# Kernel optimization log

Hardware: AMD Instinct MI355X
Metric: run time of the kernel (lower is better)

The kernel has to match this reference:

```python
import jax, jax.numpy as jnp
import numpy as np

NUM_HEADS = 8
LN_EPS = 1e-5

def setup_inputs() -> dict:
    key = jax.random.key(0)
    ks = jax.random.split(key, 8)
    B, C, H, W = 2, 512, 64, 64
    dim = C
    s = 1.0 / np.sqrt(dim)
    return {
        "pet_feat": jax.random.normal(ks[0], (B, C, H, W), jnp.float32),
        "ct_feat": jax.random.normal(ks[1], (B, C, H, W), jnp.float32),
        "Wq": jax.random.normal(ks[2], (dim, dim), jnp.float32) * s,
        "Wk": jax.random.normal(ks[3], (dim, dim), jnp.float32) * s,
        "Wv": jax.random.normal(ks[4], (dim, dim), jnp.float32) * s,
        "Wp": jax.random.normal(ks[5], (dim, dim), jnp.float32) * s,
        "bp": jnp.zeros((dim,), jnp.float32),
        "gamma": jnp.ones((dim,), jnp.float32),
        "beta": jnp.zeros((dim,), jnp.float32),
    }

def reference(pet_feat, ct_feat, Wq, Wk, Wv, Wp, bp, gamma, beta):
    B, C, H, W = pet_feat.shape
    L = H * W
    nh = NUM_HEADS
    hd = C // nh
    scale = hd ** (-0.5)
    # b c h w -> b (h w) c
    pet_seq = pet_feat.reshape(B, C, L).transpose(0, 2, 1)
    ct_seq = ct_feat.reshape(B, C, L).transpose(0, 2, 1)
    # linear projections (torch Linear: x @ W.T), split heads: b l (h d) -> b h l d
    q = (pet_seq @ Wq.T).reshape(B, L, nh, hd).transpose(0, 2, 1, 3)
    k = (ct_seq @ Wk.T).reshape(B, L, nh, hd).transpose(0, 2, 1, 3)
    v = (ct_seq @ Wv.T).reshape(B, L, nh, hd).transpose(0, 2, 1, 3)
    attn = jnp.einsum('bhld,bhmd->bhlm', q, k) * scale
    attn = jax.nn.softmax(attn, axis=-1)
    x = jnp.einsum('bhlm,bhmd->bhld', attn, v)
    # b h l d -> b l (h d)
    x = x.transpose(0, 2, 1, 3).reshape(B, L, C)
    x = x @ Wp.T + bp
    x = pet_seq + x
    # LayerNorm over channel dim
    mu = jnp.mean(x, axis=-1, keepdims=True)
    var = jnp.mean(jnp.square(x - mu), axis=-1, keepdims=True)
    x = (x - mu) * jax.lax.rsqrt(var + LN_EPS) * gamma + beta
    # b (h w) c -> b c h w
    return x.transpose(0, 2, 1).reshape(B, C, H, W)
```

## Files before the change

### kernel.cpp

```cpp
#include <hip/hip_runtime.h>

#define B_ 2
#define C_ 512
#define L_ 4096
#define NH 8
#define HD 64

typedef short bf16x8 __attribute__((ext_vector_type(8)));
typedef float f32x4 __attribute__((ext_vector_type(4)));
typedef unsigned short u16;
typedef unsigned short u16x8 __attribute__((ext_vector_type(8)));

static __device__ __forceinline__ u16 f2bf(float f) {
    union { float f; unsigned u; } v; v.f = f;
    unsigned u = v.u;
    u += 0x7fff + ((u >> 16) & 1);
    return (u16)(u >> 16);
}

static __device__ __forceinline__ unsigned cvtpk(float lo, float hi) {
    unsigned r;
    asm("v_cvt_pk_bf16_f32 %0, %1, %2" : "=v"(r) : "v"(lo), "v"(hi));
    return r;
}

__global__ __launch_bounds__(256) void transpose_conv_kernel(
        const float* __restrict__ pet, const float* __restrict__ ct,
        u16* __restrict__ petT, u16* __restrict__ ctT) {
    __shared__ float tile[64][65];
    int z  = blockIdx.z;
    int b  = z >> 1;
    const float* src = (z & 1) ? ct : pet;
    u16* dst         = (z & 1) ? ctT : petT;
    int c0 = blockIdx.y * 64;
    int l0 = blockIdx.x * 64;
    int t  = threadIdx.x;
    int i  = t >> 2;
    int jc = (t & 3) * 16;
    const float* sp = src + ((size_t)(b * C_ + c0 + i)) * L_ + l0 + jc;
#pragma unroll
    for (int p = 0; p < 4; ++p) {
        float4 v = *(const float4*)(sp + p * 4);
        tile[i][jc + p * 4 + 0] = v.x;
        tile[i][jc + p * 4 + 1] = v.y;
        tile[i][jc + p * 4 + 2] = v.z;
        tile[i][jc + p * 4 + 3] = v.w;
    }
    __syncthreads();
    int cc = (t & 3) * 16;
    u16* dp = dst + ((size_t)(b * L_ + l0 + i)) * C_ + c0 + cc;
    u16x8 o0, o1;
#pragma unroll
    for (int q = 0; q < 8; ++q) o0[q] = f2bf(tile[cc + q][i]);
#pragma unroll
    for (int q = 0; q < 8; ++q) o1[q] = f2bf(tile[cc + 8 + q][i]);
    *(u16x8*)(dp)     = o0;
    *(u16x8*)(dp + 8) = o1;
}

__global__ __launch_bounds__(256) void f2bf4_kernel(
        const float* __restrict__ s0, const float* __restrict__ s1,
        const float* __restrict__ s2, const float* __restrict__ s3,
        u16* __restrict__ d0, u16* __restrict__ d1,
        u16* __restrict__ d2, u16* __restrict__ d3) {
    const int n = 512 * 512;
    int idx = blockIdx.x * blockDim.x + threadIdx.x;
    int stride = gridDim.x * blockDim.x;
    for (int i = idx; i < n; i += stride) {
        d0[i] = f2bf(s0[i]);
        d1[i] = f2bf(s1[i]);
        d2[i] = f2bf(s2[i]);
        d3[i] = f2bf(s3[i]);
    }
}

__global__ __launch_bounds__(256) void gemm_nt_kernel(
        const u16* __restrict__ A, const u16* __restrict__ Bt,
        u16* __restrict__ Cm, int M, int N, int K,
        size_t aZ, size_t btZ, size_t cZ) {
    __shared__ u16 Al[64][72];
    __shared__ u16 Bl[64][72];
    A  += (size_t)blockIdx.z * aZ;
    Bt += (size_t)blockIdx.z * btZ;
    Cm += (size_t)blockIdx.z * cZ;
    int m0 = blockIdx.x * 64;
    int n0 = blockIdx.y * 64;
    int t = threadIdx.x;
    int w = t >> 6, lane = t & 63, ll = lane & 15, lh = lane >> 4;
    int moff = (w & 1) * 32, noff = (w >> 1) * 32;
    f32x4 acc[2][2] = {};
    int srow  = t >> 2;
    int skoff = (t & 3) * 16;
    const u16* Ap = A  + (size_t)(m0 + srow) * K + skoff;
    const u16* Bp = Bt + (size_t)(n0 + srow) * K + skoff;
    for (int kb = 0; kb < K; kb += 64) {
        u16x8 a0 = *(const u16x8*)(Ap + kb);
        u16x8 a1 = *(const u16x8*)(Ap + kb + 8);
        u16x8 b0 = *(const u16x8*)(Bp + kb);
        u16x8 b1 = *(const u16x8*)(Bp + kb + 8);
        *(u16x8*)&Al[srow][skoff]     = a0;
        *(u16x8*)&Al[srow][skoff + 8] = a1;
        *(u16x8*)&Bl[srow][skoff]     = b0;
        *(u16x8*)&Bl[srow][skoff + 8] = b1;
        __syncthreads();
#pragma unroll
        for (int kc = 0; kc < 2; ++kc) {
            bf16x8 af[2], bfr[2];
#pragma unroll
            for (int mf = 0; mf < 2; ++mf)
                af[mf] = *(const bf16x8*)&Al[moff + mf * 16 + ll][kc * 32 + lh * 8];
#pragma unroll
            for (int nf = 0; nf < 2; ++nf)
                bfr[nf] = *(const bf16x8*)&Bl[noff + nf * 16 + ll][kc * 32 + lh * 8];
#pragma unroll
            for (int mf = 0; mf < 2; ++mf)
#pragma unroll
                for (int nf = 0; nf < 2; ++nf)
                    acc[mf][nf] = __builtin_amdgcn_mfma_f32_16x16x32_bf16(
                        af[mf], bfr[nf], acc[mf][nf], 0, 0, 0);
        }
        __syncthreads();
    }
#pragma unroll
    for (int mf = 0; mf < 2; ++mf)
#pragma unroll
        for (int nf = 0; nf < 2; ++nf)
#pragma unroll
            for (int r = 0; r < 4; ++r) {
                int row = m0 + moff + mf * 16 + lh * 4 + r;
                int col = n0 + noff + nf * 16 + ll;
                Cm[(size_t)row * N + col] = f2bf(acc[mf][nf][r]);
            }
}

__global__ __launch_bounds__(256) void attn_kernel(
        const u16* __restrict__ q, const u16* __restrict__ k,
        const u16* __restrict__ vt, u16* __restrict__ X) {
    __shared__ u16 Kl[2][64][76];
    __shared__ u16 Vl[2][64][76];
    int l0 = blockIdx.x * 128;
    int h  = blockIdx.y;
    int b  = blockIdx.z;
    int t = threadIdx.x;
    int w = t >> 6, lane = t & 63, ll = lane & 15, lh = lane >> 4;
    const float C1 = 0.125f * 1.44269504088896340736f;
    const float M0 = 16.0f;

    bf16x8 qf[2][2];
#pragma unroll
    for (int u = 0; u < 2; ++u) {
        const u16* qp = q + ((size_t)(b * L_ + l0 + w * 32 + u * 16 + ll)) * C_
                          + h * HD + lh * 8;
        qf[u][0] = *(const bf16x8*)qp;
        qf[u][1] = *(const bf16x8*)(qp + 32);
    }
    int krow[4];
#pragma unroll
    for (int nf = 0; nf < 4; ++nf)
        krow[nf] = 32 * (nf & 1) + 4 * (nf >> 1) + 8 * (ll >> 2) + (ll & 3);

    int srow = t >> 2;
    int soff = (t & 3) * 16;
    const u16* kp = k  + ((size_t)(b * L_ + srow)) * C_ + h * HD + soff;
    const u16* vp = vt + ((size_t)(b * C_ + h * HD + srow)) * L_ + soff;

    u16x8 ka0 = *(const u16x8*)(kp);
    u16x8 ka1 = *(const u16x8*)(kp + 8);
    u16x8 va0 = *(const u16x8*)(vp);
    u16x8 va1 = *(const u16x8*)(vp + 8);
    *(u16x8*)&Kl[0][srow][soff]     = ka0;
    *(u16x8*)&Kl[0][srow][soff + 8] = ka1;
    *(u16x8*)&Vl[0][srow][soff]     = va0;
    *(u16x8*)&Vl[0][srow][soff + 8] = va1;
    kp += (size_t)64 * C_;
    vp += 64;

    f32x4 o[4][2] = {};
    float l_run[2] = {0.f, 0.f};

    int cur = 0;
    const int NT = L_ / 64;
    for (int tile = 0; tile < NT; ++tile) {
        __syncthreads();
        const bool pre = (tile < NT - 1);
        if (pre) {
            ka0 = *(const u16x8*)(kp);
            ka1 = *(const u16x8*)(kp + 8);
            va0 = *(const u16x8*)(vp);
            va1 = *(const u16x8*)(vp + 8);
            kp += (size_t)64 * C_;
            vp += 64;
        }
        bf16x8 kf[4][2], vf[4][2];
#pragma unroll
        for (int nf = 0; nf < 4; ++nf) {
            kf[nf][0] = *(const bf16x8*)&Kl[cur][krow[nf]][lh * 8];
            kf[nf][1] = *(const bf16x8*)&Kl[cur][krow[nf]][32 + lh * 8];
        }
#pragma unroll
        for (int df = 0; df < 4; ++df) {
            vf[df][0] = *(const bf16x8*)&Vl[cur][df * 16 + ll][lh * 8];
            vf[df][1] = *(const bf16x8*)&Vl[cur][df * 16 + ll][32 + lh * 8];
        }

        f32x4 s[2][4] = {};
#pragma unroll
        for (int kc = 0; kc < 2; ++kc)
#pragma unroll
            for (int nf = 0; nf < 4; ++nf)
#pragma unroll
                for (int u = 0; u < 2; ++u)
                    s[u][nf] = __builtin_amdgcn_mfma_f32_16x16x32_bf16(
                        kf[nf][kc], qf[u][kc], s[u][nf], 0, 0, 0);

        union { unsigned uu[4]; bf16x8 v; } pb[2][2];
#pragma unroll
        for (int u = 0; u < 2; ++u) {
            float ts = 0.f;
#pragma unroll
            for (int nf = 0; nf < 4; ++nf)
#pragma unroll
                for (int r = 0; r < 4; ++r) {
                    float pv = __builtin_amdgcn_exp2f(fmaf(s[u][nf][r], C1, -M0));
                    s[u][nf][r] = pv;
                    ts += pv;
                }
            l_run[u] += ts;
#pragma unroll
            for (int kc = 0; kc < 2; ++kc) {
                pb[kc][u].uu[0] = cvtpk(s[u][kc][0],     s[u][kc][1]);
                pb[kc][u].uu[1] = cvtpk(s[u][kc][2],     s[u][kc][3]);
                pb[kc][u].uu[2] = cvtpk(s[u][kc + 2][0], s[u][kc + 2][1]);
                pb[kc][u].uu[3] = cvtpk(s[u][kc + 2][2], s[u][kc + 2][3]);
            }
        }
#pragma unroll
        for (int kc = 0; kc < 2; ++kc)
#pragma unroll
            for (int df = 0; df < 4; ++df)
#pragma unroll
                for (int u = 0; u < 2; ++u)
                    o[df][u] = __builtin_amdgcn_mfma_f32_16x16x32_bf16(
                        vf[df][kc], pb[kc][u].v, o[df][u], 0, 0, 0);

        if (pre) {
            int nxt = cur ^ 1;
            *(u16x8*)&Kl[nxt][srow][soff]     = ka0;
            *(u16x8*)&Kl[nxt][srow][soff + 8] = ka1;
            *(u16x8*)&Vl[nxt][srow][soff]     = va0;
            *(u16x8*)&Vl[nxt][srow][soff + 8] = va1;
            cur = nxt;
        }
    }

#pragma unroll
    for (int u = 0; u < 2; ++u) {
        l_run[u] += __shfl_xor(l_run[u], 16, 64);
        l_run[u] += __shfl_xor(l_run[u], 32, 64);
    }
#pragma unroll
    for (int u = 0; u < 2; ++u) {
        float inv = 1.f / l_run[u];
        u16* xp = X + ((size_t)(b * L_ + l0 + w * 32 + u * 16 + ll)) * C_
                    + h * HD + 4 * lh;
#pragma unroll
        for (int df = 0; df < 4; ++df) {
            union { unsigned uu[2]; } pk;
            pk.uu[0] = cvtpk(o[df][u][0] * inv, o[df][u][1] * inv);
            pk.uu[1] = cvtpk(o[df][u][2] * inv, o[df][u][3] * inv);
            *(uint2*)(xp + df * 16) = *(uint2*)pk.uu;
        }
    }
}

__global__ __launch_bounds__(256) void outln_kernel(
        const u16* __restrict__ X, const u16* __restrict__ Wpb,
        const float* __restrict__ bp, const float* __restrict__ gamma,
        const float* __restrict__ beta, const float* __restrict__ pet,
        float* __restrict__ out) {
    __shared__ u16 Al[16][520];
    __shared__ float red[16][4][2];
    int g0 = blockIdx.x * 16;
    int b  = g0 >> 12;
    int l0 = g0 & (L_ - 1);
    int t = threadIdx.x;
    int w = t >> 6, lane = t & 63, ll = lane & 15, lh = lane >> 4;
    {
        int row  = t >> 4;
        int koff = (t & 15) * 32;
        const u16* xp = X + ((size_t)(g0 + row)) * C_ + koff;
#pragma unroll
        for (int p = 0; p < 4; ++p)
            *(u16x8*)&Al[row][koff + p * 8] = *(const u16x8*)(xp + p * 8);
    }
    __syncthreads();
    int nbase = w * 128;
    f32x4 acc[8] = {};
    for (int kc = 0; kc < 16; ++kc) {
        bf16x8 af = *(const bf16x8*)&Al[ll][kc * 32 + lh * 8];
#pragma unroll
        for (int nf = 0; nf < 8; ++nf) {
            int c = nbase + nf * 16 + ll;
            bf16x8 bfr = *(const bf16x8*)(Wpb + (size_t)c * C_ + kc * 32 + lh * 8);
            acc[nf] = __builtin_amdgcn_mfma_f32_16x16x32_bf16(af, bfr, acc[nf], 0, 0, 0);
        }
    }
    float psum[4] = {}, psq[4] = {};
#pragma unroll
    for (int nf = 0; nf < 8; ++nf) {
        int c = nbase + nf * 16 + ll;
        float bias = bp[c];
#pragma unroll
        for (int r = 0; r < 4; ++r) {
            int l = l0 + lh * 4 + r;
            float v = acc[nf][r] + bias + pet[((size_t)(b * C_ + c)) * L_ + l];
            acc[nf][r] = v;
            psum[r] += v;
            psq[r]  += v * v;
        }
    }
#pragma unroll
    for (int x = 1; x < 16; x <<= 1)
#pragma unroll
        for (int r = 0; r < 4; ++r) {
            psum[r] += __shfl_xor(psum[r], x, 64);
            psq[r]  += __shfl_xor(psq[r], x, 64);
        }
    if (ll == 0) {
#pragma unroll
        for (int r = 0; r < 4; ++r) {
            red[lh * 4 + r][w][0] = psum[r];
            red[lh * 4 + r][w][1] = psq[r];
        }
    }
    __syncthreads();
#pragma unroll
    for (int r = 0; r < 4; ++r) {
        int row = lh * 4 + r;
        float s  = red[row][0][0] + red[row][1][0] + red[row][2][0] + red[row][3][0];
        float sq = red[row][0][1] + red[row][1][1] + red[row][2][1] + red[row][3][1];
        float mean = s * (1.f / 512.f);
        float var  = sq * (1.f / 512.f) - mean * mean;
        float rs = rsqrtf(var + 1e-5f);
        int l = l0 + row;
#pragma unroll
        for (int nf = 0; nf < 8; ++nf) {
            int c = nbase + nf * 16 + ll;
            float v = (acc[nf][r] - mean) * rs * gamma[c] + beta[c];
            out[((size_t)(b * C_ + c)) * L_ + l] = v;
        }
    }
}

extern "C" void kernel_launch(void* const* d_in, const int* in_sizes, int n_in,
                              void* d_out, int out_size, void* d_ws, size_t ws_size,
                              hipStream_t stream) {
    const float* pet   = (const float*)d_in[0];
    const float* ct    = (const float*)d_in[1];
    const float* Wq    = (const float*)d_in[2];
    const float* Wk    = (const float*)d_in[3];
    const float* Wv    = (const float*)d_in[4];
    const float* Wp    = (const float*)d_in[5];
    const float* bp    = (const float*)d_in[6];
    const float* gamma = (const float*)d_in[7];
    const float* beta  = (const float*)d_in[8];
    float* out = (float*)d_out;

    char* ws = (char*)d_ws;
    const size_t SZ = (size_t)B_ * L_ * C_ * 2;
    const size_t NE = (size_t)B_ * L_ * C_;
    u16* petT = (u16*)(ws);
    u16* ctT  = (u16*)(ws + SZ);
    u16* qb   = (u16*)(ws + 2 * SZ);
    u16* kb   = (u16*)(ws + 3 * SZ);
    u16* vtb  = (u16*)(ws + 4 * SZ);
    u16* wqb  = (u16*)(ws + 5 * SZ);
    u16* wkb  = wqb + 512 * 512;
    u16* wvb  = wkb + 512 * 512;
    u16* wpb  = wvb + 512 * 512;
    (void)ctT; (void)kb; (void)wkb;

    dim3 tb(256);
    transpose_conv_kernel<<<dim3(L_ / 64, C_ / 64, 2 * B_), tb, 0, stream>>>(
        pet, ct, petT, ctT);
    f2bf4_kernel<<<dim3(256), tb, 0, stream>>>(Wq, Wk, Wv, Wp, wqb, wkb, wvb, wpb);

    gemm_nt_kernel<<<dim3((B_ * L_) / 64, C_ / 64, 2), tb, 0, stream>>>(
        petT, wqb, qb, B_ * L_, C_, C_,
        NE, (size_t)512 * 512, NE);
    gemm_nt_kernel<<<dim3(C_ / 64, L_ / 64, B_), tb, 0, stream>>>(
        wvb, ctT, vtb, C_, L_, C_,
        0, (size_t)L_ * C_, (size_t)C_ * L_);

    u16* Xb = petT;
    attn_kernel<<<dim3(L_ / 128, NH, B_), tb, 0, stream>>>(qb, kb, vtb, Xb);

    outln_kernel<<<dim3((B_ * L_) / 16), tb, 0, stream>>>(
        Xb, wpb, bp, gamma, beta, pet, out);
}
```

Measured before the change: 188.5 us.

## Split attention KV range across two blocks and merge partials in output LayerNorm

The attention grid is doubled so each block handles half of the key/value sequence. Each half writes an unnormalized bf16 partial output plus per-row softmax denominators. Because the softmax uses a fixed max offset, the output-projection/LayerNorm kernel can merge the halves by adding them and dividing by the summed denominators. This gives the attention launch more blocks to fill the GPU, at the cost of an extra partial-output buffer (reusing the ctT workspace), extra memory traffic, and one more bf16 rounding step. The V shared-memory row padding also changes from 76 to 72.

```diff
diff --git a/kernel.cpp b/kernel.cpp
--- a/kernel.cpp
+++ b/kernel.cpp
@@ -16,6 +16,11 @@
     unsigned u = v.u;
     u += 0x7fff + ((u >> 16) & 1);
     return (u16)(u >> 16);
+}
+
+static __device__ __forceinline__ float bf2f(u16 h) {
+    union { unsigned u; float f; } v; v.u = ((unsigned)h) << 16;
+    return v.f;
 }
 
 static __device__ __forceinline__ unsigned cvtpk(float lo, float hi) {
@@ -135,16 +140,22 @@
 
 __global__ __launch_bounds__(256) void attn_kernel(
         const u16* __restrict__ q, const u16* __restrict__ k,
-        const u16* __restrict__ vt, u16* __restrict__ X) {
+        const u16* __restrict__ vt, u16* __restrict__ Xp,
+        float* __restrict__ lp) {
     __shared__ u16 Kl[2][64][76];
-    __shared__ u16 Vl[2][64][76];
+    __shared__ u16 Vl[2][64][72];
     int l0 = blockIdx.x * 128;
     int h  = blockIdx.y;
-    int b  = blockIdx.z;
+    int z  = blockIdx.z;
+    int b  = z >> 1;
+    int split = z & 1;
     int t = threadIdx.x;
     int w = t >> 6, lane = t & 63, ll = lane & 15, lh = lane >> 4;
     const float C1 = 0.125f * 1.44269504088896340736f;
     const float M0 = 16.0f;
+    const int NT = L_ / 64;
+    const int t0 = split * (NT / 2);
+    const size_t NE = (size_t)B_ * L_ * C_;
 
     bf16x8 qf[2][2];
 #pragma unroll
@@ -161,8 +172,8 @@
 
     int srow = t >> 2;
     int soff = (t & 3) * 16;
-    const u16* kp = k  + ((size_t)(b * L_ + srow)) * C_ + h * HD + soff;
-    const u16* vp = vt + ((size_t)(b * C_ + h * HD + srow)) * L_ + soff;
+    const u16* kp = k  + ((size_t)(b * L_ + t0 * 64 + srow)) * C_ + h * HD + soff;
+    const u16* vp = vt + ((size_t)(b * C_ + h * HD + srow)) * L_ + t0 * 64 + soff;
 
     u16x8 ka0 = *(const u16x8*)(kp);
     u16x8 ka1 = *(const u16x8*)(kp + 8);
@@ -179,10 +190,10 @@
     float l_run[2] = {0.f, 0.f};
 
     int cur = 0;
-    const int NT = L_ / 64;
-    for (int tile = 0; tile < NT; ++tile) {
+    const int NLOC = NT / 2;
+    for (int tile = 0; tile < NLOC; ++tile) {
         __syncthreads();
-        const bool pre = (tile < NT - 1);
+        const bool pre = (tile < NLOC - 1);
         if (pre) {
             ka0 = *(const u16x8*)(kp);
             ka1 = *(const u16x8*)(kp + 8);
@@ -258,16 +269,18 @@
         l_run[u] += __shfl_xor(l_run[u], 16, 64);
         l_run[u] += __shfl_xor(l_run[u], 32, 64);
     }
+    u16* Xs = Xp + (size_t)split * NE;
 #pragma unroll
     for (int u = 0; u < 2; ++u) {
-        float inv = 1.f / l_run[u];
-        u16* xp = X + ((size_t)(b * L_ + l0 + w * 32 + u * 16 + ll)) * C_
-                    + h * HD + 4 * lh;
+        int row = l0 + w * 32 + u * 16 + ll;
+        if (lh == 0)
+            lp[((size_t)(split * B_ + b) * NH + h) * L_ + row] = l_run[u];
+        u16* xp = Xs + ((size_t)(b * L_ + row)) * C_ + h * HD + 4 * lh;
 #pragma unroll
         for (int df = 0; df < 4; ++df) {
             union { unsigned uu[2]; } pk;
-            pk.uu[0] = cvtpk(o[df][u][0] * inv, o[df][u][1] * inv);
-            pk.uu[1] = cvtpk(o[df][u][2] * inv, o[df][u][3] * inv);
+            pk.uu[0] = cvtpk(o[df][u][0], o[df][u][1]);
+            pk.uu[1] = cvtpk(o[df][u][2], o[df][u][3]);
             *(uint2*)(xp + df * 16) = *(uint2*)pk.uu;
         }
     }
@@ -277,9 +290,11 @@
         const u16* __restrict__ X, const u16* __restrict__ Wpb,
         const float* __restrict__ bp, const float* __restrict__ gamma,
         const float* __restrict__ beta, const float* __restrict__ pet,
-        float* __restrict__ out) {
+        const float* __restrict__ lp, float* __restrict__ out) {
     __shared__ u16 Al[16][520];
     __shared__ float red[16][4][2];
+    const size_t NE  = (size_t)B_ * L_ * C_;
+    const size_t NLP = (size_t)B_ * NH * L_;
     int g0 = blockIdx.x * 16;
     int b  = g0 >> 12;
     int l0 = g0 & (L_ - 1);
@@ -288,10 +303,23 @@
     {
         int row  = t >> 4;
         int koff = (t & 15) * 32;
-        const u16* xp = X + ((size_t)(g0 + row)) * C_ + koff;
-#pragma unroll
-        for (int p = 0; p < 4; ++p)
-            *(u16x8*)&Al[row][koff + p * 8] = *(const u16x8*)(xp + p * 8);
+        int h    = koff >> 6;
+        int labs = l0 + row;
+        float lsum = lp[((size_t)b * NH + h) * L_ + labs]
+                   + lp[NLP + ((size_t)b * NH + h) * L_ + labs];
+        float linv = 1.f / lsum;
+        const u16* x1 = X +      ((size_t)(g0 + row)) * C_ + koff;
+        const u16* x2 = X + NE + ((size_t)(g0 + row)) * C_ + koff;
+#pragma unroll
+        for (int p = 0; p < 4; ++p) {
+            u16x8 v1 = *(const u16x8*)(x1 + p * 8);
+            u16x8 v2 = *(const u16x8*)(x2 + p * 8);
+            u16x8 o8;
+#pragma unroll
+            for (int j = 0; j < 8; ++j)
+                o8[j] = f2bf((bf2f(v1[j]) + bf2f(v2[j])) * linv);
+            *(u16x8*)&Al[row][koff + p * 8] = o8;
+        }
     }
     __syncthreads();
     int nbase = w * 128;
@@ -367,18 +395,21 @@
     float* out = (float*)d_out;
 
     char* ws = (char*)d_ws;
-    const size_t SZ = (size_t)B_ * L_ * C_ * 2;
-    const size_t NE = (size_t)B_ * L_ * C_;
+    const size_t SZ  = (size_t)B_ * L_ * C_ * 2;
+    const size_t NE  = (size_t)B_ * L_ * C_;
+    const size_t WSZ = (size_t)512 * 512;
     u16* petT = (u16*)(ws);
     u16* ctT  = (u16*)(ws + SZ);
     u16* qb   = (u16*)(ws + 2 * SZ);
     u16* kb   = (u16*)(ws + 3 * SZ);
     u16* vtb  = (u16*)(ws + 4 * SZ);
     u16* wqb  = (u16*)(ws + 5 * SZ);
-    u16* wkb  = wqb + 512 * 512;
-    u16* wvb  = wkb + 512 * 512;
-    u16* wpb  = wvb + 512 * 512;
-    (void)ctT; (void)kb; (void)wkb;
+    u16* wkb  = wqb + WSZ;
+    u16* wvb  = wkb + WSZ;
+    u16* wpb  = wvb + WSZ;
+    float* lpb = (float*)(ws + 5 * SZ + 4 * WSZ * 2);
+    u16* X2   = (u16*)((char*)lpb + 2ull * B_ * NH * L_ * 4);
+    (void)kb;
 
     dim3 tb(256);
     transpose_conv_kernel<<<dim3(L_ / 64, C_ / 64, 2 * B_), tb, 0, stream>>>(
@@ -387,14 +418,16 @@
 
     gemm_nt_kernel<<<dim3((B_ * L_) / 64, C_ / 64, 2), tb, 0, stream>>>(
         petT, wqb, qb, B_ * L_, C_, C_,
-        NE, (size_t)512 * 512, NE);
+        NE, WSZ, NE);
     gemm_nt_kernel<<<dim3(C_ / 64, L_ / 64, B_), tb, 0, stream>>>(
         wvb, ctT, vtb, C_, L_, C_,
         0, (size_t)L_ * C_, (size_t)C_ * L_);
 
-    u16* Xb = petT;
-    attn_kernel<<<dim3(L_ / 128, NH, B_), tb, 0, stream>>>(qb, kb, vtb, Xb);
+    u16* X1 = petT;
+    (void)X2;
+    attn_kernel<<<dim3(L_ / 128, NH, 2 * B_), tb, 0, stream>>>(
+        qb, kb, vtb, X1, lpb);
 
     outln_kernel<<<dim3((B_ * L_) / 16), tb, 0, stream>>>(
-        Xb, wpb, bp, gamma, beta, pet, out);
-}
+        X1, wpb, bp, gamma, beta, pet, lpb, out);
+}
```

New measurement: 179.2 us. 4.9% less time.
